# Kernel tuning notes

Measured on AMD Instinct MI355X. Metric: run time of the kernel, lower is better.

## Reference

```python
import jax, jax.numpy as jnp
import numpy as np
import math

B, N, D, H = 2, 64, 256, 8
DK = D // H


def setup_inputs() -> dict:
    key = jax.random.key(0)
    ks = jax.random.split(key, 12)
    s = 1.0 / math.sqrt(D)
    inp = {
        "state": jax.random.normal(ks[0], (B, N, N, D), dtype=jnp.float32),
        "mask": jnp.zeros((B, N, N, N), dtype=bool),
        "W_lk": jax.random.normal(ks[1], (D, D), dtype=jnp.float32) * s,
        "b_lk": jnp.zeros((D,), dtype=jnp.float32),
        "W_rk": jax.random.normal(ks[2], (D, D), dtype=jnp.float32) * s,
        "b_rk": jnp.zeros((D,), dtype=jnp.float32),
        "W_lv": jax.random.normal(ks[3], (D, D), dtype=jnp.float32) * s,
        "b_lv": jnp.zeros((D,), dtype=jnp.float32),
        "W_rv": jax.random.normal(ks[4], (D, D), dtype=jnp.float32) * s,
        "b_rv": jnp.zeros((D,), dtype=jnp.float32),
        "W_o": jax.random.normal(ks[5], (D, D), dtype=jnp.float32) * s,
        "b_o": jnp.zeros((D,), dtype=jnp.float32),
    }
    return inp


def _proj(x, W, b):
    # torch nn.Linear: x @ W.T + b, then view to heads
    y = jnp.einsum('bxyd,ed->bxye', x, W) + b
    return y.reshape(B, N, N, H, DK)


def reference(state, mask, W_lk, b_lk, W_rk, b_rk, W_lv, b_lv, W_rv, b_rv, W_o, b_o):
    left_k = _proj(state, W_lk, b_lk)   # [B,N,N,H,DK]
    right_k = _proj(state, W_rk, b_rk)
    left_v = _proj(state, W_lv, b_lv)
    right_v = _proj(state, W_rv, b_rv)

    # triangle-style scores over node triples (x, a, y): [B,N,N,N,H]
    scores = jnp.einsum('bxahd,bayhd->bxayh', left_k, right_k) / math.sqrt(DK)
    scores = jnp.where(mask[..., None], jnp.float32(-1000.0), scores)
    att = jax.nn.softmax(scores, axis=2)  # softmax over intermediate node a

    # val[b,x,a,y,h,d] = left_v[b,x,a,h,d] * right_v[b,a,y,h,d] (materialized as in torch)
    val = jnp.einsum('bxahd,bayhd->bxayhd', left_v, right_v)
    x = jnp.einsum('bxayh,bxayhd->bxyhd', att, val)  # sum over a
    x = x.reshape(B, N, N, D)
    return jnp.einsum('bxyd,ed->bxye', x, W_o) + b_o
```

## Files before the change

kernel.cpp:

```cpp
#include <hip/hip_runtime.h>

#define B 2
#define N 64
#define D 256
#define H 8
#define DK 32
#define M (B * N * N)

typedef __attribute__((ext_vector_type(8))) short bf16x8;
typedef __attribute__((ext_vector_type(4))) float f32x4;
typedef __attribute__((ext_vector_type(2))) float f32x2;

#define PROJ_ELEMS (2097152)

__device__ __forceinline__ ushort f2b(float f) {
    union { float f; unsigned u; } v; v.f = f;
    unsigned r = v.u + 0x7fffu + ((v.u >> 16) & 1u);
    return (ushort)(r >> 16);
}
__device__ __forceinline__ float b2f(ushort u) {
    union { unsigned u; float f; } v; v.u = ((unsigned)u) << 16; return v.f;
}
__device__ __forceinline__ f32x2 up2(unsigned u) {
    union { unsigned u; float f; } lo, hi;
    lo.u = u << 16; hi.u = u & 0xffff0000u;
    f32x2 r; r.x = lo.f; r.y = hi.f; return r;
}

__device__ __forceinline__ void glds16(const ushort* g, ushort* l) {
    __builtin_amdgcn_global_load_lds(
        (const __attribute__((address_space(1))) unsigned int*)g,
        (__attribute__((address_space(3))) unsigned int*)l, 16, 0, 0);
}

__global__ __launch_bounds__(256) void cast_all(const float* __restrict__ state,
                                                const float* __restrict__ W_lk, const float* __restrict__ W_rk,
                                                const float* __restrict__ W_lv, const float* __restrict__ W_rv,
                                                const float* __restrict__ W_o,
                                                const float* __restrict__ b_lk, const float* __restrict__ b_rk,
                                                const float* __restrict__ b_lv, const float* __restrict__ b_rv,
                                                const float* __restrict__ b_o,
                                                ushort* __restrict__ state_bf,
                                                ushort* __restrict__ Wcat,
                                                float* __restrict__ bias_cat) {
    const int gid = blockIdx.x * 256 + threadIdx.x;
    const float* Ws[5] = {W_lk, W_rk, W_lv, W_rv, W_o};
    const float* bs[5] = {b_lk, b_rk, b_lv, b_rv, b_o};

    if (gid < 1280) bias_cat[gid] = bs[gid >> 8][gid & 255];

    if (gid < 524288) {
        float4 v = *(const float4*)&state[(size_t)gid * 4];
        ushort4 o = {f2b(v.x), f2b(v.y), f2b(v.z), f2b(v.w)};
        *(ushort4*)&state_bf[(size_t)gid * 4] = o;
    } else {
        int u = gid - 524288;
        int row = u >> 6;
        int k4 = (u & 63) * 4;
        const float* W = Ws[row >> 8];
        float4 v = *(const float4*)&W[(size_t)(row & 255) * 256 + k4];
        ushort4 o = {f2b(v.x), f2b(v.y), f2b(v.z), f2b(v.w)};
        *(ushort4*)&Wcat[(size_t)row * 256 + k4] = o;
    }
}

template <int BF16OUT, int RELAYOUT, int BM>
__global__ __launch_bounds__(256) void gemm_mfma(const ushort* __restrict__ A,
                                                 const ushort* __restrict__ Bw,
                                                 const float* __restrict__ bias,
                                                 void* __restrict__ Cv, int ldc) {
    constexpr int IR = BM / 32;
    __shared__ __align__(16) ushort As[2][2][BM * 32];
    __shared__ __align__(16) ushort Bs[2][2][128 * 32];
    const int tid = threadIdx.x;
    const int lane = tid & 63;
    const int wave = tid >> 6;
    const int wm = (wave & 1) * (BM / 2);
    const int wn = (wave >> 1) * 64;
    const int row0 = blockIdx.x * BM;
    const int col0 = blockIdx.y * 128;

    const int lr = lane >> 2;
    const int lkq = (lane & 3) * 8;

    const int arow = (BM == 128) ? (wave * 32) : (wave * 16);
    const ushort* gA0 = A + (size_t)(row0 + arow + lr) * 256 + lkq;
    const ushort* gA1 = gA0 + 16 * 256;
    const ushort* gB0 = Bw + (size_t)(col0 + wave * 32 + lr) * 256 + lkq;
    const ushort* gB1 = gB0 + 16 * 256;

    const int fr = lane & 15;
    const int fk = (lane >> 4) * 8;

    f32x4 acc[IR][4] = {};

    auto stage2 = [&](int grp) {
        const int buf = grp & 1;
#pragma unroll
        for (int p = 0; p < 2; ++p) {
            const int ko = (grp * 2 + p) * 32;
            glds16(gA0 + ko, &As[buf][p][arow * 32]);
            if (BM == 128) glds16(gA1 + ko, &As[buf][p][(arow + 16) * 32]);
            glds16(gB0 + ko, &Bs[buf][p][(wave * 32) * 32]);
            glds16(gB1 + ko, &Bs[buf][p][(wave * 32 + 16) * 32]);
        }
    };

    stage2(0);
    __syncthreads();

    for (int it = 0; it < 4; ++it) {
        if (it < 3) stage2(it + 1);
        const int buf = it & 1;
#pragma unroll
        for (int p = 0; p < 2; ++p) {
            bf16x8 af[IR], bf[4];
#pragma unroll
            for (int i = 0; i < IR; ++i)
                af[i] = *(const bf16x8*)&As[buf][p][(wm + i * 16 + fr) * 32 + fk];
#pragma unroll
            for (int j = 0; j < 4; ++j)
                bf[j] = *(const bf16x8*)&Bs[buf][p][(wn + j * 16 + fr) * 32 + fk];
#pragma unroll
            for (int i = 0; i < IR; ++i)
#pragma unroll
                for (int j = 0; j < 4; ++j)
                    acc[i][j] = __builtin_amdgcn_mfma_f32_16x16x32_bf16(af[i], bf[j], acc[i][j], 0, 0, 0);
        }
        __syncthreads();
    }

#pragma unroll
    for (int j = 0; j < 4; ++j) {
        const int col = col0 + wn + j * 16 + (lane & 15);
        const float bv = bias[col];
#pragma unroll
        for (int i = 0; i < IR; ++i) {
            const int rbase = row0 + wm + i * 16 + (lane >> 4) * 4;
#pragma unroll
            for (int r = 0; r < 4; ++r) {
                float o = acc[i][j][r] + bv;
                if (RELAYOUT) {
                    const int row = rbase + r;
                    const int bb = row >> 12, rr = row & 4095;
                    const int proj = col >> 8, hh = (col >> 5) & 7, dk = col & 31;
                    ((ushort*)Cv)[(size_t)proj * PROJ_ELEMS +
                                  ((size_t)(bb * 8 + hh) * 4096 + rr) * 32 + dk] = f2b(o);
                } else if (BF16OUT) {
                    ((ushort*)Cv)[(size_t)(rbase + r) * ldc + col] = f2b(o);
                } else {
                    ((float*)Cv)[(size_t)(rbase + r) * ldc + col] = o;
                }
            }
        }
    }
}

__global__ __launch_bounds__(512, 2) void fused_attn(const ushort* __restrict__ P,
                                                     const unsigned char* __restrict__ mask,
                                                     ushort* __restrict__ xbuf) {
    __shared__ __align__(16) ushort RVb[32 * 512];
    __shared__ __align__(16) float atts[32 * 16 * 20];
    __shared__ float mstate[16 * 20];
    __shared__ float alphas[16 * 20];

    const int bh = blockIdx.z;
    const int b = bh >> 3, h = bh & 7;
    const int x0 = blockIdx.x * 16, y0 = blockIdx.y * 16;
    const int tid = threadIdx.x;
    const int lane = tid & 63, wave = tid >> 6;

    const size_t HB = (size_t)bh * 4096 * 32;
    const ushort* PLK = P + HB;
    const ushort* PRK = P + (size_t)1 * PROJ_ELEMS + HB;
    const ushort* PLV = P + (size_t)2 * PROJ_ELEMS + HB;
    const ushort* PRV = P + (size_t)3 * PROJ_ELEMS + HB;

    const int gy = lane >> 2;
    const int du = lane & 3;
    const int sx = tid >> 4, sy = tid & 15;
    if (tid < 256) mstate[sx * 20 + sy] = -3.0e38f;

    const int sa = lane >> 2, soct = lane & 3;
    const int a4 = wave * 4;

    const ushort* lvb0 = PLV + ((size_t)(x0 + wave * 2) * 64) * 32 + du * 8;
    const ushort* lvb1 = lvb0 + 64 * 32;

    f32x2 acc[2][4] = {};
    float lacc[2] = {0.0f, 0.0f};
    const float scale = 0.17677669529663687f;

    for (int c = 0; c < 2; ++c) {
        const int ac = c * 32;
        __syncthreads();

#pragma unroll
        for (int k = 0; k < 4; ++k)
            glds16(PRV + ((size_t)(ac + a4 + k) * 64 + y0 + sa) * 32 + soct * 8,
                   &RVb[(a4 + k) * 512]);

        uint4 lvp[4][2];
#pragma unroll
        for (int s = 0; s < 4; ++s) {
            lvp[s][0] = *(const uint4*)(lvb0 + (ac + s) * 32);
            lvp[s][1] = *(const uint4*)(lvb1 + (ac + s) * 32);
        }

        {
            const int fr = lane & 15, fk = (lane >> 4) * 8;
            const int yq = lane & 15, xq = (lane >> 4) * 4;
#pragma unroll
            for (int aw = 0; aw < 4; ++aw) {
                const int a = wave * 4 + aw;
                bf16x8 af = *(const bf16x8*)&PLK[((size_t)(x0 + fr) * 64 + ac + a) * 32 + fk];
                bf16x8 bf = *(const bf16x8*)&PRK[((size_t)(ac + a) * 64 + y0 + fr) * 32 + fk];
                f32x4 s = {};
                s = __builtin_amdgcn_mfma_f32_16x16x32_bf16(af, bf, s, 0, 0, 0);
                float4 ov;
                float* op = (float*)&ov;
#pragma unroll
                for (int rr = 0; rr < 4; ++rr) {
                    float sv = s[rr] * scale;
                    if (mask[((size_t)(b * N + x0 + xq + rr) * N + ac + a) * N + y0 + yq])
                        sv = -1000.0f;
                    op[rr] = sv;
                }
                *(float4*)&atts[(a * 16 + yq) * 20 + xq] = ov;
            }
        }
        __syncthreads();

        if (tid < 256) {
            float mc = -3.0e38f;
#pragma unroll
            for (int a = 0; a < 32; ++a) mc = fmaxf(mc, atts[(a * 16 + sy) * 20 + sx]);
            const float mold = mstate[sx * 20 + sy];
            const float mnew = fmaxf(mold, mc);
            mstate[sx * 20 + sy] = mnew;
            alphas[sx * 20 + sy] = __expf(mold - mnew);
        }
        __syncthreads();

        float mn[2];
#pragma unroll
        for (int i = 0; i < 2; ++i) {
            const int x = wave * 2 + i;
            const float av = alphas[x * 20 + gy];
            mn[i] = mstate[x * 20 + gy];
            lacc[i] *= av;
#pragma unroll
            for (int q = 0; q < 4; ++q) acc[i][q] *= av;
        }

        {
            const unsigned* RV32 = (const unsigned*)RVb;
#pragma unroll
            for (int a = 0; a < 32; ++a) {
                const uint4 lv0 = lvp[a & 3][0];
                const uint4 lv1 = lvp[a & 3][1];
                if (a < 28) {
                    lvp[a & 3][0] = *(const uint4*)(lvb0 + (ac + a + 4) * 32);
                    lvp[a & 3][1] = *(const uint4*)(lvb1 + (ac + a + 4) * 32);
                }
                const uint4 rvw = *(const uint4*)&RV32[a * 256 + gy * 16 + du * 4];
                const float2 w2 = *(const float2*)&atts[(a * 16 + gy) * 20 + wave * 2];
                const float w0 = __expf(w2.x - mn[0]);
                const float w1 = __expf(w2.y - mn[1]);
                lacc[0] += w0;
                lacc[1] += w1;
                const f32x2 rv0 = up2(rvw.x), rv1 = up2(rvw.y);
                const f32x2 rv2 = up2(rvw.z), rv3 = up2(rvw.w);
                acc[0][0] += (up2(lv0.x) * w0) * rv0;
                acc[0][1] += (up2(lv0.y) * w0) * rv1;
                acc[0][2] += (up2(lv0.z) * w0) * rv2;
                acc[0][3] += (up2(lv0.w) * w0) * rv3;
                acc[1][0] += (up2(lv1.x) * w1) * rv0;
                acc[1][1] += (up2(lv1.y) * w1) * rv1;
                acc[1][2] += (up2(lv1.z) * w1) * rv2;
                acc[1][3] += (up2(lv1.w) * w1) * rv3;
            }
        }
    }

#pragma unroll
    for (int i = 0; i < 2; ++i) {
        const int x = wave * 2 + i;
        const float il = 1.0f / lacc[i];
        ushort o[8] __attribute__((aligned(16)));
#pragma unroll
        for (int q = 0; q < 4; ++q) {
            o[2 * q]     = f2b(acc[i][q].x * il);
            o[2 * q + 1] = f2b(acc[i][q].y * il);
        }
        *(uint4*)&xbuf[(((size_t)b * N + x0 + x) * N + y0 + gy) * D + h * DK + du * 8] =
            *(const uint4*)o;
    }
}

extern "C" void kernel_launch(void* const* d_in, const int* in_sizes, int n_in,
                              void* d_out, int out_size, void* d_ws, size_t ws_size,
                              hipStream_t stream) {
    const float* state = (const float*)d_in[0];
    const unsigned char* mask = (const unsigned char*)d_in[1];
    const float* W_lk = (const float*)d_in[2];
    const float* b_lk = (const float*)d_in[3];
    const float* W_rk = (const float*)d_in[4];
    const float* b_rk = (const float*)d_in[5];
    const float* W_lv = (const float*)d_in[6];
    const float* b_lv = (const float*)d_in[7];
    const float* W_rv = (const float*)d_in[8];
    const float* b_rv = (const float*)d_in[9];
    const float* W_o = (const float*)d_in[10];
    const float* b_o = (const float*)d_in[11];
    float* out = (float*)d_out;

    char* ws = (char*)d_ws;
    ushort* P_bf = (ushort*)ws;
    ws += (size_t)4 * PROJ_ELEMS * 2;
    float* bias_cat = (float*)ws;
    ws += 1280 * 4;
    ushort* state_bf = (ushort*)ws;
    ws += (size_t)M * D * 2;
    ushort* Wcat = (ushort*)ws;
    ws += (size_t)1280 * 256 * 2;
    ushort* xbuf_bf = (ushort*)ws;

    cast_all<<<2368, 256, 0, stream>>>(state, W_lk, W_rk, W_lv, W_rv, W_o,
                                       b_lk, b_rk, b_lv, b_rv, b_o,
                                       state_bf, Wcat, bias_cat);
    gemm_mfma<1, 1, 128><<<dim3(M / 128, 8), 256, 0, stream>>>(state_bf, Wcat, bias_cat, P_bf, 1024);
    fused_attn<<<dim3(4, 4, B * H), 512, 0, stream>>>(P_bf, mask, xbuf_bf);
    gemm_mfma<0, 0, 64><<<dim3(M / 64, 2), 256, 0, stream>>>(xbuf_bf, Wcat + 1024 * 256, bias_cat + 1024, out, 256);
}
```

Before: 123.7 us.

## Double-buffer LK/RK/LV/RV tiles in LDS with async prefetch across 16-wide chunks

```diff
diff --git a/kernel.cpp b/kernel.cpp
--- a/kernel.cpp
+++ b/kernel.cpp
@@ -159,8 +159,11 @@
 __global__ __launch_bounds__(512, 2) void fused_attn(const ushort* __restrict__ P,
                                                      const unsigned char* __restrict__ mask,
                                                      ushort* __restrict__ xbuf) {
-    __shared__ __align__(16) ushort RVb[32 * 512];
-    __shared__ __align__(16) float atts[32 * 16 * 20];
+    __shared__ __align__(16) ushort LKb[2][16 * 512];
+    __shared__ __align__(16) ushort RKb[2][16 * 512];
+    __shared__ __align__(16) ushort LVb[2][16 * 512];
+    __shared__ __align__(16) ushort RVb[2][16 * 512];
+    __shared__ __align__(16) float atts[16 * 16 * 20];
     __shared__ float mstate[16 * 20];
     __shared__ float alphas[16 * 20];
 
@@ -178,69 +181,89 @@
 
     const int gy = lane >> 2;
     const int du = lane & 3;
+    const int fr = lane & 15, fk = (lane >> 4) * 8;
+    const int yq = lane & 15, xq = (lane >> 4) * 4;
     const int sx = tid >> 4, sy = tid & 15;
     if (tid < 256) mstate[sx * 20 + sy] = -3.0e38f;
 
     const int sa = lane >> 2, soct = lane & 3;
-    const int a4 = wave * 4;
-
-    const ushort* lvb0 = PLV + ((size_t)(x0 + wave * 2) * 64) * 32 + du * 8;
-    const ushort* lvb1 = lvb0 + 64 * 32;
+    const int r2 = wave * 2;
 
     f32x2 acc[2][4] = {};
     float lacc[2] = {0.0f, 0.0f};
     const float scale = 0.17677669529663687f;
 
-    for (int c = 0; c < 2; ++c) {
-        const int ac = c * 32;
+    unsigned char mreg[2][4];
+
+#define STAGE(ac_, buf_)                                                                      \
+    do {                                                                                      \
+        glds16(PLK + ((size_t)(x0 + r2) * 64 + (ac_) + sa) * 32 + soct * 8,                   \
+               &LKb[buf_][r2 * 512]);                                                         \
+        glds16(PLK + ((size_t)(x0 + r2 + 1) * 64 + (ac_) + sa) * 32 + soct * 8,               \
+               &LKb[buf_][(r2 + 1) * 512]);                                                   \
+        glds16(PLV + ((size_t)(x0 + r2) * 64 + (ac_) + sa) * 32 + soct * 8,                   \
+               &LVb[buf_][r2 * 512]);                                                         \
+        glds16(PLV + ((size_t)(x0 + r2 + 1) * 64 + (ac_) + sa) * 32 + soct * 8,               \
+               &LVb[buf_][(r2 + 1) * 512]);                                                   \
+        glds16(PRK + ((size_t)((ac_) + r2) * 64 + y0 + sa) * 32 + soct * 8,                   \
+               &RKb[buf_][r2 * 512]);                                                         \
+        glds16(PRK + ((size_t)((ac_) + r2 + 1) * 64 + y0 + sa) * 32 + soct * 8,               \
+               &RKb[buf_][(r2 + 1) * 512]);                                                   \
+        glds16(PRV + ((size_t)((ac_) + r2) * 64 + y0 + sa) * 32 + soct * 8,                   \
+               &RVb[buf_][r2 * 512]);                                                         \
+        glds16(PRV + ((size_t)((ac_) + r2 + 1) * 64 + y0 + sa) * 32 + soct * 8,               \
+               &RVb[buf_][(r2 + 1) * 512]);                                                   \
+    } while (0)
+
+#define MLOAD(ac_)                                                                            \
+    do {                                                                                      \
+        _Pragma("unroll") for (int aw = 0; aw < 2; ++aw)                                      \
+        _Pragma("unroll") for (int rr = 0; rr < 4; ++rr)                                      \
+            mreg[aw][rr] = mask[((size_t)(b * N + x0 + xq + rr) * N + (ac_) + wave * 2 + aw)  \
+                                    * N + y0 + yq];                                           \
+    } while (0)
+
+    STAGE(0, 0);
+    MLOAD(0);
+
+    for (int c = 0; c < 4; ++c) {
+        const int cur = c & 1;
         __syncthreads();
 
 #pragma unroll
-        for (int k = 0; k < 4; ++k)
-            glds16(PRV + ((size_t)(ac + a4 + k) * 64 + y0 + sa) * 32 + soct * 8,
-                   &RVb[(a4 + k) * 512]);
-
-        uint4 lvp[4][2];
-#pragma unroll
-        for (int s = 0; s < 4; ++s) {
-            lvp[s][0] = *(const uint4*)(lvb0 + (ac + s) * 32);
-            lvp[s][1] = *(const uint4*)(lvb1 + (ac + s) * 32);
-        }
-
-        {
-            const int fr = lane & 15, fk = (lane >> 4) * 8;
-            const int yq = lane & 15, xq = (lane >> 4) * 4;
-#pragma unroll
-            for (int aw = 0; aw < 4; ++aw) {
-                const int a = wave * 4 + aw;
-                bf16x8 af = *(const bf16x8*)&PLK[((size_t)(x0 + fr) * 64 + ac + a) * 32 + fk];
-                bf16x8 bf = *(const bf16x8*)&PRK[((size_t)(ac + a) * 64 + y0 + fr) * 32 + fk];
-                f32x4 s = {};
-                s = __builtin_amdgcn_mfma_f32_16x16x32_bf16(af, bf, s, 0, 0, 0);
-                float4 ov;
-                float* op = (float*)&ov;
-#pragma unroll
-                for (int rr = 0; rr < 4; ++rr) {
-                    float sv = s[rr] * scale;
-                    if (mask[((size_t)(b * N + x0 + xq + rr) * N + ac + a) * N + y0 + yq])
-                        sv = -1000.0f;
-                    op[rr] = sv;
-                }
-                *(float4*)&atts[(a * 16 + yq) * 20 + xq] = ov;
+        for (int aw = 0; aw < 2; ++aw) {
+            const int al = wave * 2 + aw;
+            bf16x8 af = *(const bf16x8*)&LKb[cur][fr * 512 + al * 32 + fk];
+            bf16x8 bf = *(const bf16x8*)&RKb[cur][al * 512 + fr * 32 + fk];
+            f32x4 s = {};
+            s = __builtin_amdgcn_mfma_f32_16x16x32_bf16(af, bf, s, 0, 0, 0);
+            float4 ov;
+            float* op = (float*)&ov;
+#pragma unroll
+            for (int rr = 0; rr < 4; ++rr) {
+                float sv = s[rr] * scale;
+                if (mreg[aw][rr]) sv = -1000.0f;
+                op[rr] = sv;
             }
+            *(float4*)&atts[(al * 16 + yq) * 20 + xq] = ov;
         }
         __syncthreads();
 
         if (tid < 256) {
             float mc = -3.0e38f;
 #pragma unroll
-            for (int a = 0; a < 32; ++a) mc = fmaxf(mc, atts[(a * 16 + sy) * 20 + sx]);
+            for (int a = 0; a < 16; ++a) mc = fmaxf(mc, atts[(a * 16 + sy) * 20 + sx]);
             const float mold = mstate[sx * 20 + sy];
             const float mnew = fmaxf(mold, mc);
             mstate[sx * 20 + sy] = mnew;
             alphas[sx * 20 + sy] = __expf(mold - mnew);
         }
         __syncthreads();
+
+        if (c < 3) {
+            STAGE((c + 1) * 16, cur ^ 1);
+            MLOAD((c + 1) * 16);
+        }
 
         float mn[2];
 #pragma unroll
@@ -254,15 +277,12 @@
         }
 
         {
-            const unsigned* RV32 = (const unsigned*)RVb;
-#pragma unroll
-            for (int a = 0; a < 32; ++a) {
-                const uint4 lv0 = lvp[a & 3][0];
-                const uint4 lv1 = lvp[a & 3][1];
-                if (a < 28) {
-                    lvp[a & 3][0] = *(const uint4*)(lvb0 + (ac + a + 4) * 32);
-                    lvp[a & 3][1] = *(const uint4*)(lvb1 + (ac + a + 4) * 32);
-                }
+            const unsigned* LV32 = (const unsigned*)&LVb[cur][0];
+            const unsigned* RV32 = (const unsigned*)&RVb[cur][0];
+#pragma unroll
+            for (int a = 0; a < 16; ++a) {
+                const uint4 lv0 = *(const uint4*)&LV32[(wave * 2) * 256 + a * 16 + du * 4];
+                const uint4 lv1 = *(const uint4*)&LV32[(wave * 2 + 1) * 256 + a * 16 + du * 4];
                 const uint4 rvw = *(const uint4*)&RV32[a * 256 + gy * 16 + du * 4];
                 const float2 w2 = *(const float2*)&atts[(a * 16 + gy) * 20 + wave * 2];
                 const float w0 = __expf(w2.x - mn[0]);
@@ -296,6 +316,8 @@
         *(uint4*)&xbuf[(((size_t)b * N + x0 + x) * N + y0 + gy) * D + h * DK + du * 8] =
             *(const uint4*)o;
     }
+#undef STAGE
+#undef MLOAD
 }
 
 extern "C" void kernel_launch(void* const* d_in, const int* in_sizes, int n_in,
```

After: 123.9 us. About the same (+0.1%).
